# Performance work log

Measured on AMD Instinct MI355X. Metric: run time of the kernel, lower is better.

Reference implementation:

```python
import jax, jax.numpy as jnp
import numpy as np

B, S, D = 2, 2048, 1024
H, HD = 16, 64          # n_heads, head_dim (H*HD == D)
E, K, F = 8, 2, 1024    # n_experts, top_k, expert hidden size
EPS = 1e-6


def setup_inputs() -> dict:
    key = jax.random.key(0)
    ks = jax.random.split(key, 10)
    g = lambda k, shape, sc: jax.random.normal(k, shape, jnp.float32) * sc
    return {
        "x": g(ks[0], (B, S, D), 1.0),
        "attn_norm_w": jnp.ones((D,), jnp.float32),
        "wq": g(ks[1], (D, D), 0.02),
        "wk": g(ks[2], (D, D), 0.02),
        "wv": g(ks[3], (D, D), 0.02),
        "wo": g(ks[4], (D, D), 0.02),
        "ffn_norm_w": jnp.ones((D,), jnp.float32),
        "router_w": g(ks[5], (D, E), 0.02),
        "w1": g(ks[6], (E, D, F), 0.02),  # gate proj per expert
        "w3": g(ks[7], (E, D, F), 0.02),  # up proj per expert
        "w2": g(ks[8], (E, F, D), 0.02),  # down proj per expert
    }


def rmsnorm(x, w):
    return x * jax.lax.rsqrt(jnp.mean(x * x, axis=-1, keepdims=True) + EPS) * w


def attention(x, wq, wk, wv, wo):
    b, s, d = x.shape
    q = (x @ wq).reshape(b, s, H, HD)
    k = (x @ wk).reshape(b, s, H, HD)
    v = (x @ wv).reshape(b, s, H, HD)
    scores = jnp.einsum("bqhd,bkhd->bhqk", q, k) / jnp.sqrt(jnp.float32(HD))
    causal = jnp.tril(jnp.ones((s, s), bool))
    scores = jnp.where(causal, scores, jnp.finfo(scores.dtype).min)
    p = jax.nn.softmax(scores, axis=-1)
    o = jnp.einsum("bhqk,bkhd->bqhd", p, v).reshape(b, s, d)
    return o @ wo


def moe_ffn(x, router_w, w1, w2, w3):
    b, s, d = x.shape
    xt = x.reshape(-1, d)                       # [T, D]
    probs = jax.nn.softmax(xt @ router_w, axis=-1)  # [T, E]
    gate, idx = jax.lax.top_k(probs, K)         # [T, K]
    gate = gate / jnp.sum(gate, axis=-1, keepdims=True)  # renormalize top-k
    T = xt.shape[0]
    combine = jnp.zeros((T, E), xt.dtype).at[jnp.arange(T)[:, None], idx].set(gate)
    out = jnp.zeros_like(xt)
    for e in range(E):  # fixed small loop over experts (dense-equivalent dispatch)
        h = jax.nn.silu(xt @ w1[e]) * (xt @ w3[e])
        out = out + combine[:, e:e + 1] * (h @ w2[e])
    return out.reshape(b, s, d)


def reference(x, attn_norm_w, wq, wk, wv, wo, ffn_norm_w, router_w, w1, w2, w3):
    # h = x + dropout(attn(norm(x)));  out = h + dropout(moe(norm(h)))  (dropout=0)
    h = x + attention(rmsnorm(x, attn_norm_w), wq, wk, wv, wo)
    return h + moe_ffn(rmsnorm(h, ffn_norm_w), router_w, w1, w2, w3)
```

## Files before the change

### kernel.cpp

```cpp
#include <hip/hip_runtime.h>
#include <cstdint>
#include <math.h>

typedef unsigned short u16;
typedef unsigned int u32;
typedef __bf16 bf16x8 __attribute__((ext_vector_type(8)));
typedef float f32x4 __attribute__((ext_vector_type(4)));

#define TBATCH 2
#define TSEQ   2048
#define TDIM   1024
#define THEADS 16
#define THDIM  64
#define TEXP   8
#define TFF    1024
#define TTOK   (TBATCH*TSEQ)
#define TPAIRS (TTOK*2)

__device__ __forceinline__ u16 f2bf(float f) {
  u32 u = __float_as_uint(f);
  u += 0x7FFFu + ((u >> 16) & 1u);
  return (u16)(u >> 16);
}
__device__ __forceinline__ float bf2f(u16 h) { return __uint_as_float(((u32)h) << 16); }

__device__ __forceinline__ void gll16(const void* g, void* l) {
  __builtin_amdgcn_global_load_lds((const __attribute__((address_space(1))) void*)g,
                                   (__attribute__((address_space(3))) void*)l, 16, 0, 0);
}
__device__ __forceinline__ bf16x8 ldsread(const void* p) { return *(const bf16x8*)p; }
__device__ __forceinline__ f32x4 mm16(bf16x8 a, bf16x8 b, f32x4 c) {
  return __builtin_amdgcn_mfma_f32_16x16x32_bf16(a, b, c, 0, 0, 0);
}
__device__ __forceinline__ f32x4 fzero() { f32x4 z = {0.f, 0.f, 0.f, 0.f}; return z; }

__global__ void split_transpose_k(const float* __restrict__ in, u16* __restrict__ outh,
                                  u16* __restrict__ outl, int R, int C) {
  __shared__ float t[32][33];
  const size_t bo = (size_t)blockIdx.z * R * C;
  const int c0 = blockIdx.x * 32, r0 = blockIdx.y * 32;
  const int tx = threadIdx.x, ty = threadIdx.y;
#pragma unroll
  for (int j = 0; j < 32; j += 8)
    t[ty + j][tx] = in[bo + (size_t)(r0 + ty + j) * C + (c0 + tx)];
  __syncthreads();
#pragma unroll
  for (int j = 0; j < 32; j += 8) {
    float v = t[tx][ty + j];
    u16 hv = f2bf(v);
    size_t o = bo + (size_t)(c0 + ty + j) * R + (r0 + tx);
    outh[o] = hv;
    if (outl != nullptr) outl[o] = f2bf(v - bf2f(hv));
  }
}

template<bool SPLIT>
__launch_bounds__(256)
__global__ void rmsnorm_k(const float* __restrict__ x, const float* __restrict__ w,
                          u16* __restrict__ oh, u16* __restrict__ ol) {
  const int t = blockIdx.x, tid = threadIdx.x;
  const float4 xv = ((const float4*)(x + (size_t)t * TDIM))[tid];
  float ss = xv.x*xv.x + xv.y*xv.y + xv.z*xv.z + xv.w*xv.w;
#pragma unroll
  for (int d = 1; d < 64; d <<= 1) ss += __shfl_xor(ss, d, 64);
  __shared__ float sp[4];
  if ((tid & 63) == 0) sp[tid >> 6] = ss;
  __syncthreads();
  const float rsc = rsqrtf((sp[0] + sp[1] + sp[2] + sp[3]) * (1.0f / TDIM) + 1e-6f);
  const float4 wv = ((const float4*)w)[tid];
  float v0 = xv.x*rsc*wv.x, v1 = xv.y*rsc*wv.y, v2 = xv.z*rsc*wv.z, v3 = xv.w*rsc*wv.w;
  u16 h0 = f2bf(v0), h1 = f2bf(v1), h2 = f2bf(v2), h3 = f2bf(v3);
  uint2 ph; ph.x = (u32)h0 | ((u32)h1 << 16); ph.y = (u32)h2 | ((u32)h3 << 16);
  *(uint2*)(oh + (size_t)t * TDIM + tid * 4) = ph;
  if (SPLIT) {
    u16 l0 = f2bf(v0 - bf2f(h0)), l1 = f2bf(v1 - bf2f(h1));
    u16 l2 = f2bf(v2 - bf2f(h2)), l3 = f2bf(v3 - bf2f(h3));
    uint2 pl; pl.x = (u32)l0 | ((u32)l1 << 16); pl.y = (u32)l2 | ((u32)l3 << 16);
    *(uint2*)(ol + (size_t)t * TDIM + tid * 4) = pl;
  }
}

template<int EPI>
__launch_bounds__(256)
__global__ void gemm_x3_k(const u16* __restrict__ Ah, const u16* __restrict__ Al,
                          const u16* __restrict__ Bth, const u16* __restrict__ Btl,
                          u16* __restrict__ outh, u16* __restrict__ outl,
                          float* __restrict__ outf, const float* __restrict__ resid,
                          int M, int N, int K) {
  __shared__ u16 sAh[128 * 32], sAl[128 * 32], sBh[64 * 32], sBl[64 * 32];
  const int tid = threadIdx.x, wid = tid >> 6, lane = tid & 63;
  const int m0 = blockIdx.x * 128, n0 = blockIdx.y * 64;
  const int wr = wid >> 1, wc = wid & 1;

  f32x4 acc[4][2];
#pragma unroll
  for (int i = 0; i < 4; i++)
#pragma unroll
    for (int j = 0; j < 2; j++) acc[i][j] = fzero();

  const int srow = tid >> 2;
  const int scol = (tid & 3) * 8;
  const size_t a0 = (size_t)(m0 + srow) * K + scol;
  const size_t a1 = (size_t)(m0 + srow + 64) * K + scol;
  const size_t b0 = (size_t)(n0 + srow) * K + scol;
  const int ldsw = wid * 1024;

  int aoffs[4], boffs[2];
#pragma unroll
  for (int mf = 0; mf < 4; mf++) aoffs[mf] = (wr*64 + mf*16 + (lane & 15)) * 64 + ((lane >> 4) * 16);
#pragma unroll
  for (int nf = 0; nf < 2; nf++) boffs[nf] = (wc*32 + nf*16 + (lane & 15)) * 64 + ((lane >> 4) * 16);

  const int nk = K >> 5;
  for (int kk = 0; kk < nk; ++kk) {
    const int ke = kk * 32;
    gll16(Ah + a0 + ke, (char*)sAh + ldsw);
    gll16(Ah + a1 + ke, (char*)sAh + 4096 + ldsw);
    gll16(Al + a0 + ke, (char*)sAl + ldsw);
    gll16(Al + a1 + ke, (char*)sAl + 4096 + ldsw);
    gll16(Bth + b0 + ke, (char*)sBh + ldsw);
    gll16(Btl + b0 + ke, (char*)sBl + ldsw);
    __syncthreads();
    bf16x8 fah[4], fal[4], fbh[2], fbl[2];
#pragma unroll
    for (int mf = 0; mf < 4; mf++) { fah[mf] = ldsread((char*)sAh + aoffs[mf]); fal[mf] = ldsread((char*)sAl + aoffs[mf]); }
#pragma unroll
    for (int nf = 0; nf < 2; nf++) { fbh[nf] = ldsread((char*)sBh + boffs[nf]); fbl[nf] = ldsread((char*)sBl + boffs[nf]); }
#pragma unroll
    for (int mf = 0; mf < 4; mf++)
#pragma unroll
      for (int nf = 0; nf < 2; nf++) {
        acc[mf][nf] = mm16(fah[mf], fbh[nf], acc[mf][nf]);
        acc[mf][nf] = mm16(fah[mf], fbl[nf], acc[mf][nf]);
        acc[mf][nf] = mm16(fal[mf], fbh[nf], acc[mf][nf]);
      }
    __syncthreads();
  }

#pragma unroll
  for (int mf = 0; mf < 4; mf++)
#pragma unroll
    for (int nf = 0; nf < 2; nf++)
#pragma unroll
      for (int r = 0; r < 4; r++) {
        const int grow = m0 + wr*64 + mf*16 + ((lane >> 4) * 4) + r;
        const int gcol = n0 + wc*32 + nf*16 + (lane & 15);
        const float v = acc[mf][nf][r];
        if (EPI == 0) {
          const size_t o = (size_t)grow * N + gcol;
          u16 hv = f2bf(v);
          outh[o] = hv; outl[o] = f2bf(v - bf2f(hv));
        } else if (EPI == 1) {
          const int b = grow >> 11, s = grow & (TSEQ - 1);
          const int hh = gcol >> 6, hd = gcol & 63;
          const size_t o = ((size_t)((b * THEADS + hh) * THDIM + hd)) * TSEQ + s;
          u16 hv = f2bf(v);
          outh[o] = hv; outl[o] = f2bf(v - bf2f(hv));
        } else {
          const size_t o = (size_t)grow * N + gcol;
          outf[o] = v + resid[o];
        }
      }
}

__launch_bounds__(256)
__global__ void flash_k(const u16* __restrict__ Qh, const u16* __restrict__ Ql,
                        const u16* __restrict__ Kh, const u16* __restrict__ Kl,
                        const u16* __restrict__ Vth, const u16* __restrict__ Vtl,
                        u16* __restrict__ Oh, u16* __restrict__ Ol) {
  __shared__ u16 sK[2][2][4096];
  __shared__ u16 sV[2][2][4096];
  __shared__ u16 sP[2][4][1024];
  const int tid = threadIdx.x, wid = tid >> 6, lane = tid & 63;
  const int qb = blockIdx.x, bh = blockIdx.y;
  const int b = bh >> 4, h = bh & 15;
  const int srow = tid >> 3;
  const int sxcol = (((lane & 7) ^ ((lane >> 3) & 7)) << 3);
  const int ldsw = wid * 1024;

  bf16x8 fqh[2], fql[2];
  {
    const size_t qbase = ((size_t)(b * TSEQ + qb * 64 + wid * 16 + (lane & 15))) * TDIM + h * 64;
#pragma unroll
    for (int kq = 0; kq < 2; kq++) {
      fqh[kq] = *(const bf16x8*)(Qh + qbase + (kq * 4 + (lane >> 4)) * 8);
      fql[kq] = *(const bf16x8*)(Ql + qbase + (kq * 4 + (lane >> 4)) * 8);
    }
  }

  f32x4 oacc[4];
  float m_run[4], l_run[4];
#pragma unroll
  for (int i = 0; i < 4; i++) { oacc[i] = fzero(); m_run[i] = -INFINITY; l_run[i] = 0.f; }

  const size_t kg0 = ((size_t)(b * TSEQ + srow)) * TDIM + h * 64 + sxcol;
  const size_t kg1 = kg0 + (size_t)32 * TDIM;
  const size_t vg0 = ((size_t)((b * THEADS + h) * THDIM + srow)) * TSEQ + sxcol;
  const size_t vg1 = vg0 + (size_t)32 * TSEQ;

  auto stage = [&](int kb, int bi) {
    const size_t ko = (size_t)kb * 64 * TDIM;
    const size_t vo = (size_t)kb * 64;
    gll16(Kh + kg0 + ko, (char*)sK[bi][0] + ldsw);
    gll16(Kh + kg1 + ko, (char*)sK[bi][0] + 4096 + ldsw);
    gll16(Kl + kg0 + ko, (char*)sK[bi][1] + ldsw);
    gll16(Kl + kg1 + ko, (char*)sK[bi][1] + 4096 + ldsw);
    gll16(Vth + vg0 + vo, (char*)sV[bi][0] + ldsw);
    gll16(Vth + vg1 + vo, (char*)sV[bi][0] + 4096 + ldsw);
    gll16(Vtl + vg0 + vo, (char*)sV[bi][1] + ldsw);
    gll16(Vtl + vg1 + vo, (char*)sV[bi][1] + 4096 + ldsw);
  };

  stage(0, 0);
  asm volatile("s_waitcnt vmcnt(0)" ::: "memory");
  __builtin_amdgcn_s_barrier();

  for (int kb = 0; kb <= qb; ++kb) {
    const int cur = kb & 1;
    if (kb < qb) stage(kb + 1, cur ^ 1);

    f32x4 sc[4];
#pragma unroll
    for (int nf = 0; nf < 4; nf++) {
      f32x4 s = fzero();
      const int krow = nf * 16 + (lane & 15);
#pragma unroll
      for (int kq = 0; kq < 2; kq++) {
        const int off = krow * 128 + (((kq * 4 + (lane >> 4)) ^ (lane & 7)) << 4);
        bf16x8 kfh = ldsread((char*)sK[cur][0] + off);
        bf16x8 kfl = ldsread((char*)sK[cur][1] + off);
        s = mm16(fqh[kq], kfh, s);
        s = mm16(fqh[kq], kfl, s);
        s = mm16(fql[kq], kfh, s);
      }
      sc[nf] = s;
    }

    const int qg = qb * 64 + wid * 16 + ((lane >> 4) * 4);
    float pm[4] = {-INFINITY, -INFINITY, -INFINITY, -INFINITY};
#pragma unroll
    for (int nf = 0; nf < 4; nf++) {
      const int kg = kb * 64 + nf * 16 + (lane & 15);
#pragma unroll
      for (int r = 0; r < 4; r++) {
        float v = sc[nf][r] * 0.125f;
        if (kg > qg + r) v = -INFINITY;
        sc[nf][r] = v;
        pm[r] = fmaxf(pm[r], v);
      }
    }
#pragma unroll
    for (int r = 0; r < 4; r++)
#pragma unroll
      for (int d = 1; d < 16; d <<= 1) pm[r] = fmaxf(pm[r], __shfl_xor(pm[r], d, 64));

    float mn[4], esc[4], rs[4];
#pragma unroll
    for (int r = 0; r < 4; r++) {
      mn[r] = fmaxf(m_run[r], pm[r]);
      esc[r] = __expf(m_run[r] - mn[r]);
      rs[r] = 0.f;
    }
#pragma unroll
    for (int nf = 0; nf < 4; nf++)
#pragma unroll
      for (int r = 0; r < 4; r++) {
        float p = __expf(sc[nf][r] - mn[r]);
        sc[nf][r] = p;
        rs[r] += p;
      }
#pragma unroll
    for (int r = 0; r < 4; r++)
#pragma unroll
      for (int d = 1; d < 16; d <<= 1) rs[r] += __shfl_xor(rs[r], d, 64);
#pragma unroll
    for (int r = 0; r < 4; r++) {
      l_run[r] = l_run[r] * esc[r] + rs[r];
      m_run[r] = mn[r];
    }
#pragma unroll
    for (int nf = 0; nf < 4; nf++)
#pragma unroll
      for (int r = 0; r < 4; r++) oacc[nf][r] *= esc[r];

#pragma unroll
    for (int nf = 0; nf < 4; nf++)
#pragma unroll
      for (int r = 0; r < 4; r++) {
        float p = sc[nf][r];
        u16 ph = f2bf(p);
        const int prow = (lane >> 4) * 4 + r;
        const int pbyte = (prow * 128 + (nf * 16 + (lane & 15)) * 2) ^ ((prow & 7) << 4);
        *(u16*)((char*)sP[0][wid] + pbyte) = ph;
        *(u16*)((char*)sP[1][wid] + pbyte) = f2bf(p - bf2f(ph));
      }

#pragma unroll
    for (int nf = 0; nf < 4; nf++) {
#pragma unroll
      for (int kq = 0; kq < 2; kq++) {
        const int prow = lane & 15;
        const int poff = prow * 128 + (((kq * 4 + (lane >> 4)) ^ (prow & 7)) << 4);
        bf16x8 pah = ldsread((char*)sP[0][wid] + poff);
        bf16x8 pal = ldsread((char*)sP[1][wid] + poff);
        const int vrow = nf * 16 + (lane & 15);
        const int voff = vrow * 128 + (((kq * 4 + (lane >> 4)) ^ (lane & 7)) << 4);
        bf16x8 vfh = ldsread((char*)sV[cur][0] + voff);
        bf16x8 vfl = ldsread((char*)sV[cur][1] + voff);
        oacc[nf] = mm16(pah, vfh, oacc[nf]);
        oacc[nf] = mm16(pah, vfl, oacc[nf]);
        oacc[nf] = mm16(pal, vfh, oacc[nf]);
      }
    }
    asm volatile("s_waitcnt vmcnt(0)" ::: "memory");
    __builtin_amdgcn_s_barrier();
  }

#pragma unroll
  for (int r = 0; r < 4; r++) {
    const float inv = 1.0f / l_run[r];
    const int t = b * TSEQ + qb * 64 + wid * 16 + ((lane >> 4) * 4) + r;
#pragma unroll
    for (int nf = 0; nf < 4; nf++) {
      const float v = oacc[nf][r] * inv;
      const size_t o = (size_t)t * TDIM + h * 64 + nf * 16 + (lane & 15);
      u16 hv = f2bf(v);
      Oh[o] = hv; Ol[o] = f2bf(v - bf2f(hv));
    }
  }
}

__launch_bounds__(256)
__global__ void router_k(const float* __restrict__ hres, const float* __restrict__ wn,
                         const float* __restrict__ rw, int* __restrict__ idx01,
                         float* __restrict__ gate01, int* __restrict__ counts) {
  const int t = blockIdx.x, tid = threadIdx.x;
  const float4 xv = ((const float4*)(hres + (size_t)t * TDIM))[tid];
  float ss = xv.x*xv.x + xv.y*xv.y + xv.z*xv.z + xv.w*xv.w;
#pragma unroll
  for (int d = 1; d < 64; d <<= 1) ss += __shfl_xor(ss, d, 64);
  __shared__ float sp[4];
  __shared__ float sacc[4][8];
  if ((tid & 63) == 0) sp[tid >> 6] = ss;
  __syncthreads();
  const float rsc = rsqrtf((sp[0]+sp[1]+sp[2]+sp[3]) * (1.0f / TDIM) + 1e-6f);
  const float4 wv = ((const float4*)wn)[tid];
  const float x0 = xv.x*rsc*wv.x, x1 = xv.y*rsc*wv.y, x2 = xv.z*rsc*wv.z, x3 = xv.w*rsc*wv.w;
  const float* rp = rw + (size_t)(tid * 4) * TEXP;
  float acc[8];
#pragma unroll
  for (int e = 0; e < 8; e++) acc[e] = x0*rp[e] + x1*rp[8+e] + x2*rp[16+e] + x3*rp[24+e];
#pragma unroll
  for (int e = 0; e < 8; e++)
#pragma unroll
    for (int d = 1; d < 64; d <<= 1) acc[e] += __shfl_xor(acc[e], d, 64);
  if ((tid & 63) == 0)
#pragma unroll
    for (int e = 0; e < 8; e++) sacc[tid >> 6][e] = acc[e];
  __syncthreads();
  if (tid == 0) {
    float lg[8];
#pragma unroll
    for (int e = 0; e < 8; e++) lg[e] = sacc[0][e] + sacc[1][e] + sacc[2][e] + sacc[3][e];
    int i1 = 0;
#pragma unroll
    for (int e = 1; e < 8; e++) if (lg[e] > lg[i1]) i1 = e;
    int i2 = (i1 == 0) ? 1 : 0;
#pragma unroll
    for (int e = 0; e < 8; e++) if (e != i1 && lg[e] > lg[i2]) i2 = e;
    const float g1 = 1.0f / (1.0f + __expf(lg[i2] - lg[i1]));
    idx01[t*2] = i1; idx01[t*2+1] = i2;
    gate01[t*2] = g1; gate01[t*2+1] = 1.0f - g1;
    atomicAdd(&counts[i1], 1);
    atomicAdd(&counts[i2], 1);
  }
}

__global__ void zero8_k(int* counts) { if (threadIdx.x < TEXP) counts[threadIdx.x] = 0; }

__global__ void offsets_k(const int* __restrict__ counts, int* __restrict__ cursor,
                          int* __restrict__ bm_e, int* __restrict__ bm_s0,
                          int* __restrict__ bm_end, int* __restrict__ n_active) {
  if (threadIdx.x != 0 || blockIdx.x != 0) return;
  int off = 0, nb = 0;
  for (int e = 0; e < TEXP; e++) {
    const int c = counts[e];
    cursor[e] = off;
    const int end = off + c;
    for (int mb = 0; mb * 128 < c; mb++) { bm_e[nb] = e; bm_s0[nb] = off + mb * 128; bm_end[nb] = end; nb++; }
    off = end;
  }
  *n_active = nb;
}

__global__ void scatter_k(const int* __restrict__ idx01, int* __restrict__ cursor,
                          int* __restrict__ slot_of, int* __restrict__ perm) {
  const int t = blockIdx.x * 256 + threadIdx.x;
  if (t >= TTOK) return;
#pragma unroll
  for (int k = 0; k < 2; k++) {
    const int e = idx01[t*2+k];
    const int slot = atomicAdd(&cursor[e], 1);
    slot_of[t*2+k] = slot;
    perm[slot] = t;
  }
}

__launch_bounds__(256)
__global__ void moe_gemm1_k(const u16* __restrict__ hn, const u16* __restrict__ w1t,
                            const u16* __restrict__ w3t, const int* __restrict__ perm,
                            const int* __restrict__ bm_e, const int* __restrict__ bm_s0,
                            const int* __restrict__ bm_end, const int* __restrict__ n_active,
                            u16* __restrict__ hbuf) {
  if ((int)blockIdx.x >= *n_active) return;
  __shared__ u16 sA[128 * 32], sB1[64 * 32], sB3[64 * 32];
  const int tid = threadIdx.x, wid = tid >> 6, lane = tid & 63;
  const int e = bm_e[blockIdx.x], slot0 = bm_s0[blockIdx.x], send = bm_end[blockIdx.x];
  const int n0 = blockIdx.y * 64;
  const int wr = wid >> 1, wc = wid & 1;
  const int srow = tid >> 2, scol = (tid & 3) * 8;
  const int sa0 = slot0 + srow, sa1 = slot0 + srow + 64;
  const int ta = (sa0 < send) ? perm[sa0] : 0;
  const int tb2 = (sa1 < send) ? perm[sa1] : 0;
  const size_t a0 = (size_t)ta * TDIM + scol;
  const size_t a1 = (size_t)tb2 * TDIM + scol;
  const size_t bb = (size_t)e * TDIM * TFF + (size_t)(n0 + srow) * TDIM + scol;
  const int ldsw = wid * 1024;
  f32x4 ac1[4][2], ac3[4][2];
#pragma unroll
  for (int i = 0; i < 4; i++)
#pragma unroll
    for (int j = 0; j < 2; j++) { ac1[i][j] = fzero(); ac3[i][j] = fzero(); }
  int aoffs[4], boffs[2];
#pragma unroll
  for (int mf = 0; mf < 4; mf++) aoffs[mf] = (wr*64 + mf*16 + (lane & 15)) * 64 + ((lane >> 4) * 16);
#pragma unroll
  for (int nf = 0; nf < 2; nf++) boffs[nf] = (wc*32 + nf*16 + (lane & 15)) * 64 + ((lane >> 4) * 16);

  for (int kk = 0; kk < 32; ++kk) {
    const int ke = kk * 32;
    gll16(hn + a0 + ke, (char*)sA + ldsw);
    gll16(hn + a1 + ke, (char*)sA + 4096 + ldsw);
    gll16(w1t + bb + ke, (char*)sB1 + ldsw);
    gll16(w3t + bb + ke, (char*)sB3 + ldsw);
    __syncthreads();
    bf16x8 fa[4], f1[2], f3[2];
#pragma unroll
    for (int mf = 0; mf < 4; mf++) fa[mf] = ldsread((char*)sA + aoffs[mf]);
#pragma unroll
    for (int nf = 0; nf < 2; nf++) { f1[nf] = ldsread((char*)sB1 + boffs[nf]); f3[nf] = ldsread((char*)sB3 + boffs[nf]); }
#pragma unroll
    for (int mf = 0; mf < 4; mf++)
#pragma unroll
      for (int nf = 0; nf < 2; nf++) {
        ac1[mf][nf] = mm16(fa[mf], f1[nf], ac1[mf][nf]);
        ac3[mf][nf] = mm16(fa[mf], f3[nf], ac3[mf][nf]);
      }
    __syncthreads();
  }

#pragma unroll
  for (int mf = 0; mf < 4; mf++)
#pragma unroll
    for (int nf = 0; nf < 2; nf++)
#pragma unroll
      for (int r = 0; r < 4; r++) {
        const int slot = slot0 + wr*64 + mf*16 + ((lane >> 4) * 4) + r;
        if (slot < send) {
          const int col = n0 + wc*32 + nf*16 + (lane & 15);
          const float z1 = ac1[mf][nf][r], z3 = ac3[mf][nf][r];
          const float hv = z1 / (1.0f + __expf(-z1)) * z3;
          hbuf[(size_t)slot * TFF + col] = f2bf(hv);
        }
      }
}

__launch_bounds__(256)
__global__ void moe_gemm2_k(const u16* __restrict__ hbuf, const u16* __restrict__ w2t,
                            const int* __restrict__ bm_e, const int* __restrict__ bm_s0,
                            const int* __restrict__ bm_end, const int* __restrict__ n_active,
                            u16* __restrict__ pout) {
  if ((int)blockIdx.x >= *n_active) return;
  __shared__ u16 sA[128 * 32], sB[64 * 32];
  const int tid = threadIdx.x, wid = tid >> 6, lane = tid & 63;
  const int e = bm_e[blockIdx.x], slot0 = bm_s0[blockIdx.x], send = bm_end[blockIdx.x];
  const int n0 = blockIdx.y * 64;
  const int wr = wid >> 1, wc = wid & 1;
  const int srow = tid >> 2, scol = (tid & 3) * 8;
  int sa0 = slot0 + srow; if (sa0 > TPAIRS - 1) sa0 = TPAIRS - 1;
  int sa1 = slot0 + srow + 64; if (sa1 > TPAIRS - 1) sa1 = TPAIRS - 1;
  const size_t a0 = (size_t)sa0 * TFF + scol;
  const size_t a1 = (size_t)sa1 * TFF + scol;
  const size_t bb = (size_t)e * TDIM * TFF + (size_t)(n0 + srow) * TFF + scol;
  const int ldsw = wid * 1024;
  f32x4 acc[4][2];
#pragma unroll
  for (int i = 0; i < 4; i++)
#pragma unroll
    for (int j = 0; j < 2; j++) acc[i][j] = fzero();
  int aoffs[4], boffs[2];
#pragma unroll
  for (int mf = 0; mf < 4; mf++) aoffs[mf] = (wr*64 + mf*16 + (lane & 15)) * 64 + ((lane >> 4) * 16);
#pragma unroll
  for (int nf = 0; nf < 2; nf++) boffs[nf] = (wc*32 + nf*16 + (lane & 15)) * 64 + ((lane >> 4) * 16);

  for (int kk = 0; kk < 32; ++kk) {
    const int ke = kk * 32;
    gll16(hbuf + a0 + ke, (char*)sA + ldsw);
    gll16(hbuf + a1 + ke, (char*)sA + 4096 + ldsw);
    gll16(w2t + bb + ke, (char*)sB + ldsw);
    __syncthreads();
    bf16x8 fa[4], fb[2];
#pragma unroll
    for (int mf = 0; mf < 4; mf++) fa[mf] = ldsread((char*)sA + aoffs[mf]);
#pragma unroll
    for (int nf = 0; nf < 2; nf++) fb[nf] = ldsread((char*)sB + boffs[nf]);
#pragma unroll
    for (int mf = 0; mf < 4; mf++)
#pragma unroll
      for (int nf = 0; nf < 2; nf++)
        acc[mf][nf] = mm16(fa[mf], fb[nf], acc[mf][nf]);
    __syncthreads();
  }

#pragma unroll
  for (int mf = 0; mf < 4; mf++)
#pragma unroll
    for (int nf = 0; nf < 2; nf++)
#pragma unroll
      for (int r = 0; r < 4; r++) {
        const int slot = slot0 + wr*64 + mf*16 + ((lane >> 4) * 4) + r;
        if (slot < send) {
          const int col = n0 + wc*32 + nf*16 + (lane & 15);
          pout[(size_t)slot * TDIM + col] = f2bf(acc[mf][nf][r]);
        }
      }
}

__launch_bounds__(256)
__global__ void combine_k(const float* __restrict__ hres, const u16* __restrict__ pout,
                          const int* __restrict__ slot_of, const float* __restrict__ gate01,
                          float* __restrict__ out) {
  const int t = blockIdx.x, tid = threadIdx.x;
  const int s0 = slot_of[t*2], s1 = slot_of[t*2+1];
  const float g0 = gate01[t*2], g1 = gate01[t*2+1];
  const float4 hv = ((const float4*)(hres + (size_t)t * TDIM))[tid];
  const uint2 u0 = *(const uint2*)(pout + (size_t)s0 * TDIM + tid * 4);
  const uint2 u1 = *(const uint2*)(pout + (size_t)s1 * TDIM + tid * 4);
  float4 o;
  o.x = hv.x + g0 * bf2f((u16)(u0.x & 0xffff)) + g1 * bf2f((u16)(u1.x & 0xffff));
  o.y = hv.y + g0 * bf2f((u16)(u0.x >> 16))    + g1 * bf2f((u16)(u1.x >> 16));
  o.z = hv.z + g0 * bf2f((u16)(u0.y & 0xffff)) + g1 * bf2f((u16)(u1.y & 0xffff));
  o.w = hv.w + g0 * bf2f((u16)(u0.y >> 16))    + g1 * bf2f((u16)(u1.y >> 16));
  ((float4*)(out + (size_t)t * TDIM))[tid] = o;
}

extern "C" void kernel_launch(void* const* d_in, const int* in_sizes, int n_in,
                              void* d_out, int out_size, void* d_ws, size_t ws_size,
                              hipStream_t stream) {
  (void)in_sizes; (void)n_in; (void)out_size; (void)ws_size;
  const float* x   = (const float*)d_in[0];
  const float* anw = (const float*)d_in[1];
  const float* wq  = (const float*)d_in[2];
  const float* wk  = (const float*)d_in[3];
  const float* wv  = (const float*)d_in[4];
  const float* wo  = (const float*)d_in[5];
  const float* fnw = (const float*)d_in[6];
  const float* rw  = (const float*)d_in[7];
  const float* w1  = (const float*)d_in[8];
  const float* w3  = (const float*)d_in[9];
  const float* w2  = (const float*)d_in[10];
  float* out = (float*)d_out;

  char* ws = (char*)d_ws;
  size_t off = 0;
  auto take = [&](size_t bytes) -> char* {
    char* p = ws + off;
    off += (bytes + 255) & ~(size_t)255;
    return p;
  };
  const size_t SZ_W = (size_t)TDIM * TDIM * sizeof(u16);
  const size_t SZ_T = (size_t)TTOK * TDIM * sizeof(u16);
  u16* wqt_h = (u16*)take(SZ_W); u16* wqt_l = (u16*)take(SZ_W);
  u16* wkt_h = (u16*)take(SZ_W); u16* wkt_l = (u16*)take(SZ_W);
  u16* wvt_h = (u16*)take(SZ_W); u16* wvt_l = (u16*)take(SZ_W);
  u16* wot_h = (u16*)take(SZ_W); u16* wot_l = (u16*)take(SZ_W);
  u16* w1t = (u16*)take((size_t)TEXP * TDIM * TFF * sizeof(u16));
  u16* w3t = (u16*)take((size_t)TEXP * TDIM * TFF * sizeof(u16));
  u16* w2t = (u16*)take((size_t)TEXP * TDIM * TFF * sizeof(u16));
  u16* xnh = (u16*)take(SZ_T); u16* xnl = (u16*)take(SZ_T);
  u16* qh  = (u16*)take(SZ_T); u16* ql  = (u16*)take(SZ_T);
  u16* kh  = (u16*)take(SZ_T); u16* kl  = (u16*)take(SZ_T);
  u16* vth = (u16*)take(SZ_T); u16* vtl = (u16*)take(SZ_T);
  float* hres = (float*)take((size_t)TTOK * TDIM * sizeof(float));
  int*   idx01  = (int*)take(TTOK * 2 * 4);
  float* gate01 = (float*)take(TTOK * 2 * 4);
  int*   slot_of = (int*)take(TTOK * 2 * 4);
  int*   perm    = (int*)take(TPAIRS * 4);
  int*   counts  = (int*)take(256);
  int*   cursor  = (int*)take(256);
  int*   bm_e    = (int*)take(96 * 4);
  int*   bm_s0   = (int*)take(96 * 4);
  int*   bm_end  = (int*)take(96 * 4);
  int*   n_act   = (int*)take(256);
  u16* oh = xnh; u16* ol = xnl;
  u16* hn = qh;
  u16* hbuf = kh;
  u16* pout = vth;

  dim3 tb32(32, 8);
  split_transpose_k<<<dim3(32, 32, 1), tb32, 0, stream>>>(wq, wqt_h, wqt_l, TDIM, TDIM);
  split_transpose_k<<<dim3(32, 32, 1), tb32, 0, stream>>>(wk, wkt_h, wkt_l, TDIM, TDIM);
  split_transpose_k<<<dim3(32, 32, 1), tb32, 0, stream>>>(wv, wvt_h, wvt_l, TDIM, TDIM);
  split_transpose_k<<<dim3(32, 32, 1), tb32, 0, stream>>>(wo, wot_h, wot_l, TDIM, TDIM);
  split_transpose_k<<<dim3(32, 32, 8), tb32, 0, stream>>>(w1, w1t, nullptr, TDIM, TFF);
  split_transpose_k<<<dim3(32, 32, 8), tb32, 0, stream>>>(w3, w3t, nullptr, TDIM, TFF);
  split_transpose_k<<<dim3(32, 32, 8), tb32, 0, stream>>>(w2, w2t, nullptr, TFF, TDIM);
  zero8_k<<<1, 64, 0, stream>>>(counts);
  rmsnorm_k<true><<<TTOK, 256, 0, stream>>>(x, anw, xnh, xnl);
  gemm_x3_k<0><<<dim3(TTOK/128, TDIM/64), 256, 0, stream>>>(xnh, xnl, wqt_h, wqt_l, qh, ql, nullptr, nullptr, TTOK, TDIM, TDIM);
  gemm_x3_k<0><<<dim3(TTOK/128, TDIM/64), 256, 0, stream>>>(xnh, xnl, wkt_h, wkt_l, kh, kl, nullptr, nullptr, TTOK, TDIM, TDIM);
  gemm_x3_k<1><<<dim3(TTOK/128, TDIM/64), 256, 0, stream>>>(xnh, xnl, wvt_h, wvt_l, vth, vtl, nullptr, nullptr, TTOK, TDIM, TDIM);
  flash_k<<<dim3(TSEQ/64, TBATCH*THEADS), 256, 0, stream>>>(qh, ql, kh, kl, vth, vtl, oh, ol);
  gemm_x3_k<2><<<dim3(TTOK/128, TDIM/64), 256, 0, stream>>>(oh, ol, wot_h, wot_l, nullptr, nullptr, hres, x, TTOK, TDIM, TDIM);
  rmsnorm_k<false><<<TTOK, 256, 0, stream>>>(hres, fnw, hn, nullptr);
  router_k<<<TTOK, 256, 0, stream>>>(hres, fnw, rw, idx01, gate01, counts);
  offsets_k<<<1, 1, 0, stream>>>(counts, cursor, bm_e, bm_s0, bm_end, n_act);
  scatter_k<<<TTOK/256, 256, 0, stream>>>(idx01, cursor, slot_of, perm);
  moe_gemm1_k<<<dim3(72, TFF/64), 256, 0, stream>>>(hn, w1t, w3t, perm, bm_e, bm_s0, bm_end, n_act, hbuf);
  moe_gemm2_k<<<dim3(72, TDIM/64), 256, 0, stream>>>(hbuf, w2t, bm_e, bm_s0, bm_end, n_act, pout);
  combine_k<<<TTOK, 256, 0, stream>>>(hres, pout, slot_of, gate01, out);
}
```

Baseline: 645.1 us.

## Process two query tiles per flash block, reverse block order, defer row-sum reduction

Each flash-attention block now handles 128 query rows as two 64-row halves that share every staged K/V tile, halving global K/V traffic per query. Blocks are launched in reverse query order so the longest causal rows start first, which should improve tail balance. The per-iteration cross-lane row-sum shuffle is replaced by per-lane partial sums reduced once at the end. The cost is half as many blocks (512), more registers for the doubled accumulators, and one fully masked half on the last K tile.

```diff
diff --git a/kernel.cpp b/kernel.cpp
--- a/kernel.cpp
+++ b/kernel.cpp
@@ -172,26 +172,30 @@
   __shared__ u16 sV[2][2][4096];
   __shared__ u16 sP[2][4][1024];
   const int tid = threadIdx.x, wid = tid >> 6, lane = tid & 63;
-  const int qb = blockIdx.x, bh = blockIdx.y;
+  const int qb = (int)(gridDim.x - 1 - blockIdx.x);
+  const int bh = blockIdx.y;
   const int b = bh >> 4, h = bh & 15;
   const int srow = tid >> 3;
   const int sxcol = (((lane & 7) ^ ((lane >> 3) & 7)) << 3);
   const int ldsw = wid * 1024;
 
-  bf16x8 fqh[2], fql[2];
-  {
-    const size_t qbase = ((size_t)(b * TSEQ + qb * 64 + wid * 16 + (lane & 15))) * TDIM + h * 64;
+  bf16x8 fqh[2][2], fql[2][2];
+#pragma unroll
+  for (int hh = 0; hh < 2; hh++) {
+    const size_t qbase = ((size_t)(b * TSEQ + qb * 128 + hh * 64 + wid * 16 + (lane & 15))) * TDIM + h * 64;
 #pragma unroll
     for (int kq = 0; kq < 2; kq++) {
-      fqh[kq] = *(const bf16x8*)(Qh + qbase + (kq * 4 + (lane >> 4)) * 8);
-      fql[kq] = *(const bf16x8*)(Ql + qbase + (kq * 4 + (lane >> 4)) * 8);
+      fqh[hh][kq] = *(const bf16x8*)(Qh + qbase + (kq * 4 + (lane >> 4)) * 8);
+      fql[hh][kq] = *(const bf16x8*)(Ql + qbase + (kq * 4 + (lane >> 4)) * 8);
     }
   }
 
-  f32x4 oacc[4];
-  float m_run[4], l_run[4];
-#pragma unroll
-  for (int i = 0; i < 4; i++) { oacc[i] = fzero(); m_run[i] = -INFINITY; l_run[i] = 0.f; }
+  f32x4 oacc[2][4];
+  float m_run[2][4], l_lane[2][4];
+#pragma unroll
+  for (int hh = 0; hh < 2; hh++)
+#pragma unroll
+    for (int i = 0; i < 4; i++) { oacc[hh][i] = fzero(); m_run[hh][i] = -INFINITY; l_lane[hh][i] = 0.f; }
 
   const size_t kg0 = ((size_t)(b * TSEQ + srow)) * TDIM + h * 64 + sxcol;
   const size_t kg1 = kg0 + (size_t)32 * TDIM;
@@ -211,105 +215,105 @@
     gll16(Vtl + vg1 + vo, (char*)sV[bi][1] + 4096 + ldsw);
   };
 
+  const int nkb = 2 * qb + 2;
   stage(0, 0);
   asm volatile("s_waitcnt vmcnt(0)" ::: "memory");
   __builtin_amdgcn_s_barrier();
 
-  for (int kb = 0; kb <= qb; ++kb) {
+  for (int kb = 0; kb < nkb; ++kb) {
     const int cur = kb & 1;
-    if (kb < qb) stage(kb + 1, cur ^ 1);
-
-    f32x4 sc[4];
-#pragma unroll
-    for (int nf = 0; nf < 4; nf++) {
-      f32x4 s = fzero();
-      const int krow = nf * 16 + (lane & 15);
-#pragma unroll
-      for (int kq = 0; kq < 2; kq++) {
-        const int off = krow * 128 + (((kq * 4 + (lane >> 4)) ^ (lane & 7)) << 4);
-        bf16x8 kfh = ldsread((char*)sK[cur][0] + off);
-        bf16x8 kfl = ldsread((char*)sK[cur][1] + off);
-        s = mm16(fqh[kq], kfh, s);
-        s = mm16(fqh[kq], kfl, s);
-        s = mm16(fql[kq], kfh, s);
-      }
-      sc[nf] = s;
-    }
-
-    const int qg = qb * 64 + wid * 16 + ((lane >> 4) * 4);
-    float pm[4] = {-INFINITY, -INFINITY, -INFINITY, -INFINITY};
-#pragma unroll
-    for (int nf = 0; nf < 4; nf++) {
-      const int kg = kb * 64 + nf * 16 + (lane & 15);
+    if (kb + 1 < nkb) stage(kb + 1, cur ^ 1);
+
+#pragma unroll
+    for (int hh = 0; hh < 2; hh++) {
+      if (kb * 64 > qb * 128 + hh * 64 + 63) continue;
+
+      f32x4 sc[4];
+#pragma unroll
+      for (int nf = 0; nf < 4; nf++) {
+        f32x4 s = fzero();
+        const int krow = nf * 16 + (lane & 15);
+#pragma unroll
+        for (int kq = 0; kq < 2; kq++) {
+          const int off = krow * 128 + (((kq * 4 + (lane >> 4)) ^ (lane & 7)) << 4);
+          bf16x8 kfh = ldsread((char*)sK[cur][0] + off);
+          bf16x8 kfl = ldsread((char*)sK[cur][1] + off);
+          s = mm16(fqh[hh][kq], kfh, s);
+          s = mm16(fqh[hh][kq], kfl, s);
+          s = mm16(fql[hh][kq], kfh, s);
+        }
+        sc[nf] = s;
+      }
+
+      const int qg = qb * 128 + hh * 64 + wid * 16 + ((lane >> 4) * 4);
+      float pm[4] = {-INFINITY, -INFINITY, -INFINITY, -INFINITY};
+#pragma unroll
+      for (int nf = 0; nf < 4; nf++) {
+        const int kg = kb * 64 + nf * 16 + (lane & 15);
+#pragma unroll
+        for (int r = 0; r < 4; r++) {
+          float v = sc[nf][r] * 0.125f;
+          if (kg > qg + r) v = -INFINITY;
+          sc[nf][r] = v;
+          pm[r] = fmaxf(pm[r], v);
+        }
+      }
+#pragma unroll
+      for (int r = 0; r < 4; r++)
+#pragma unroll
+        for (int d = 1; d < 16; d <<= 1) pm[r] = fmaxf(pm[r], __shfl_xor(pm[r], d, 64));
+
+      float mn[4], esc[4];
 #pragma unroll
       for (int r = 0; r < 4; r++) {
-        float v = sc[nf][r] * 0.125f;
-        if (kg > qg + r) v = -INFINITY;
-        sc[nf][r] = v;
-        pm[r] = fmaxf(pm[r], v);
-      }
-    }
-#pragma unroll
-    for (int r = 0; r < 4; r++)
-#pragma unroll
-      for (int d = 1; d < 16; d <<= 1) pm[r] = fmaxf(pm[r], __shfl_xor(pm[r], d, 64));
-
-    float mn[4], esc[4], rs[4];
-#pragma unroll
-    for (int r = 0; r < 4; r++) {
-      mn[r] = fmaxf(m_run[r], pm[r]);
-      esc[r] = __expf(m_run[r] - mn[r]);
-      rs[r] = 0.f;
-    }
-#pragma unroll
-    for (int nf = 0; nf < 4; nf++)
-#pragma unroll
-      for (int r = 0; r < 4; r++) {
-        float p = __expf(sc[nf][r] - mn[r]);
-        sc[nf][r] = p;
-        rs[r] += p;
-      }
-#pragma unroll
-    for (int r = 0; r < 4; r++)
-#pragma unroll
-      for (int d = 1; d < 16; d <<= 1) rs[r] += __shfl_xor(rs[r], d, 64);
-#pragma unroll
-    for (int r = 0; r < 4; r++) {
-      l_run[r] = l_run[r] * esc[r] + rs[r];
-      m_run[r] = mn[r];
-    }
-#pragma unroll
-    for (int nf = 0; nf < 4; nf++)
-#pragma unroll
-      for (int r = 0; r < 4; r++) oacc[nf][r] *= esc[r];
-
-#pragma unroll
-    for (int nf = 0; nf < 4; nf++)
-#pragma unroll
-      for (int r = 0; r < 4; r++) {
-        float p = sc[nf][r];
-        u16 ph = f2bf(p);
-        const int prow = (lane >> 4) * 4 + r;
-        const int pbyte = (prow * 128 + (nf * 16 + (lane & 15)) * 2) ^ ((prow & 7) << 4);
-        *(u16*)((char*)sP[0][wid] + pbyte) = ph;
-        *(u16*)((char*)sP[1][wid] + pbyte) = f2bf(p - bf2f(ph));
-      }
-
-#pragma unroll
-    for (int nf = 0; nf < 4; nf++) {
-#pragma unroll
-      for (int kq = 0; kq < 2; kq++) {
-        const int prow = lane & 15;
-        const int poff = prow * 128 + (((kq * 4 + (lane >> 4)) ^ (prow & 7)) << 4);
-        bf16x8 pah = ldsread((char*)sP[0][wid] + poff);
-        bf16x8 pal = ldsread((char*)sP[1][wid] + poff);
-        const int vrow = nf * 16 + (lane & 15);
-        const int voff = vrow * 128 + (((kq * 4 + (lane >> 4)) ^ (lane & 7)) << 4);
-        bf16x8 vfh = ldsread((char*)sV[cur][0] + voff);
-        bf16x8 vfl = ldsread((char*)sV[cur][1] + voff);
-        oacc[nf] = mm16(pah, vfh, oacc[nf]);
-        oacc[nf] = mm16(pah, vfl, oacc[nf]);
-        oacc[nf] = mm16(pal, vfh, oacc[nf]);
+        mn[r] = fmaxf(m_run[hh][r], pm[r]);
+        esc[r] = __expf(m_run[hh][r] - mn[r]);
+        m_run[hh][r] = mn[r];
+      }
+      float ls[4] = {0.f, 0.f, 0.f, 0.f};
+#pragma unroll
+      for (int nf = 0; nf < 4; nf++)
+#pragma unroll
+        for (int r = 0; r < 4; r++) {
+          float p = __expf(sc[nf][r] - mn[r]);
+          sc[nf][r] = p;
+          ls[r] += p;
+        }
+#pragma unroll
+      for (int r = 0; r < 4; r++) l_lane[hh][r] = l_lane[hh][r] * esc[r] + ls[r];
+#pragma unroll
+      for (int nf = 0; nf < 4; nf++)
+#pragma unroll
+        for (int r = 0; r < 4; r++) oacc[hh][nf][r] *= esc[r];
+
+#pragma unroll
+      for (int nf = 0; nf < 4; nf++)
+#pragma unroll
+        for (int r = 0; r < 4; r++) {
+          float p = sc[nf][r];
+          u16 ph = f2bf(p);
+          const int prow = (lane >> 4) * 4 + r;
+          const int pbyte = (prow * 128 + (nf * 16 + (lane & 15)) * 2) ^ ((prow & 7) << 4);
+          *(u16*)((char*)sP[0][wid] + pbyte) = ph;
+          *(u16*)((char*)sP[1][wid] + pbyte) = f2bf(p - bf2f(ph));
+        }
+
+#pragma unroll
+      for (int nf = 0; nf < 4; nf++) {
+#pragma unroll
+        for (int kq = 0; kq < 2; kq++) {
+          const int prow = lane & 15;
+          const int poff = prow * 128 + (((kq * 4 + (lane >> 4)) ^ (prow & 7)) << 4);
+          bf16x8 pah = ldsread((char*)sP[0][wid] + poff);
+          bf16x8 pal = ldsread((char*)sP[1][wid] + poff);
+          const int vrow = nf * 16 + (lane & 15);
+          const int voff = vrow * 128 + (((kq * 4 + (lane >> 4)) ^ (lane & 7)) << 4);
+          bf16x8 vfh = ldsread((char*)sV[cur][0] + voff);
+          bf16x8 vfl = ldsread((char*)sV[cur][1] + voff);
+          oacc[hh][nf] = mm16(pah, vfh, oacc[hh][nf]);
+          oacc[hh][nf] = mm16(pah, vfl, oacc[hh][nf]);
+          oacc[hh][nf] = mm16(pal, vfh, oacc[hh][nf]);
+        }
       }
     }
     asm volatile("s_waitcnt vmcnt(0)" ::: "memory");
@@ -317,17 +321,22 @@
   }
 
 #pragma unroll
-  for (int r = 0; r < 4; r++) {
-    const float inv = 1.0f / l_run[r];
-    const int t = b * TSEQ + qb * 64 + wid * 16 + ((lane >> 4) * 4) + r;
-#pragma unroll
-    for (int nf = 0; nf < 4; nf++) {
-      const float v = oacc[nf][r] * inv;
-      const size_t o = (size_t)t * TDIM + h * 64 + nf * 16 + (lane & 15);
-      u16 hv = f2bf(v);
-      Oh[o] = hv; Ol[o] = f2bf(v - bf2f(hv));
+  for (int hh = 0; hh < 2; hh++)
+#pragma unroll
+    for (int r = 0; r < 4; r++) {
+      float lt = l_lane[hh][r];
+#pragma unroll
+      for (int d = 1; d < 16; d <<= 1) lt += __shfl_xor(lt, d, 64);
+      const float inv = 1.0f / lt;
+      const int t = b * TSEQ + qb * 128 + hh * 64 + wid * 16 + ((lane >> 4) * 4) + r;
+#pragma unroll
+      for (int nf = 0; nf < 4; nf++) {
+        const float v = oacc[hh][nf][r] * inv;
+        const size_t o = (size_t)t * TDIM + h * 64 + nf * 16 + (lane & 15);
+        u16 hv = f2bf(v);
+        Oh[o] = hv; Ol[o] = f2bf(v - bf2f(hv));
+      }
     }
-  }
 }
 
 __launch_bounds__(256)
@@ -621,7 +630,7 @@
   gemm_x3_k<0><<<dim3(TTOK/128, TDIM/64), 256, 0, stream>>>(xnh, xnl, wqt_h, wqt_l, qh, ql, nullptr, nullptr, TTOK, TDIM, TDIM);
   gemm_x3_k<0><<<dim3(TTOK/128, TDIM/64), 256, 0, stream>>>(xnh, xnl, wkt_h, wkt_l, kh, kl, nullptr, nullptr, TTOK, TDIM, TDIM);
   gemm_x3_k<1><<<dim3(TTOK/128, TDIM/64), 256, 0, stream>>>(xnh, xnl, wvt_h, wvt_l, vth, vtl, nullptr, nullptr, TTOK, TDIM, TDIM);
-  flash_k<<<dim3(TSEQ/64, TBATCH*THEADS), 256, 0, stream>>>(qh, ql, kh, kl, vth, vtl, oh, ol);
+  flash_k<<<dim3(TSEQ/128, TBATCH*THEADS), 256, 0, stream>>>(qh, ql, kh, kl, vth, vtl, oh, ol);
   gemm_x3_k<2><<<dim3(TTOK/128, TDIM/64), 256, 0, stream>>>(oh, ol, wot_h, wot_l, nullptr, nullptr, hres, x, TTOK, TDIM, TDIM);
   rmsnorm_k<false><<<TTOK, 256, 0, stream>>>(hres, fnw, hn, nullptr);
   router_k<<<TTOK, 256, 0, stream>>>(hres, fnw, rw, idx01, gate01, counts);
```

Result: faster. 621.0 us (-3.7%).

## Load flash K/V fragments directly from global, reverse block order, defer row-sum reduction

Applied to the files above, without the earlier changes.

The flash attention kernel stops staging K and V tiles through double-buffered shared memory with barriers. Each wave now reads its MFMA fragments straight from global memory and relies on the cache for reuse across the four waves. Query blocks are also launched in reverse order so the longest causal blocks start first, and the softmax row-sum cross-lane reduction moves out of the loop to a single final reduction. This removes LDS traffic and per-iteration barriers, but it costs more global/L2 loads per wave with no explicit prefetch, so load latency may be exposed.

```diff
diff --git a/kernel.cpp b/kernel.cpp
--- a/kernel.cpp
+++ b/kernel.cpp
@@ -168,15 +168,11 @@
                         const u16* __restrict__ Kh, const u16* __restrict__ Kl,
                         const u16* __restrict__ Vth, const u16* __restrict__ Vtl,
                         u16* __restrict__ Oh, u16* __restrict__ Ol) {
-  __shared__ u16 sK[2][2][4096];
-  __shared__ u16 sV[2][2][4096];
   __shared__ u16 sP[2][4][1024];
   const int tid = threadIdx.x, wid = tid >> 6, lane = tid & 63;
-  const int qb = blockIdx.x, bh = blockIdx.y;
+  const int qb = (int)(gridDim.x - 1 - blockIdx.x);
+  const int bh = blockIdx.y;
   const int b = bh >> 4, h = bh & 15;
-  const int srow = tid >> 3;
-  const int sxcol = (((lane & 7) ^ ((lane >> 3) & 7)) << 3);
-  const int ldsw = wid * 1024;
 
   bf16x8 fqh[2], fql[2];
   {
@@ -189,46 +185,34 @@
   }
 
   f32x4 oacc[4];
-  float m_run[4], l_run[4];
-#pragma unroll
-  for (int i = 0; i < 4; i++) { oacc[i] = fzero(); m_run[i] = -INFINITY; l_run[i] = 0.f; }
-
-  const size_t kg0 = ((size_t)(b * TSEQ + srow)) * TDIM + h * 64 + sxcol;
-  const size_t kg1 = kg0 + (size_t)32 * TDIM;
-  const size_t vg0 = ((size_t)((b * THEADS + h) * THDIM + srow)) * TSEQ + sxcol;
-  const size_t vg1 = vg0 + (size_t)32 * TSEQ;
-
-  auto stage = [&](int kb, int bi) {
-    const size_t ko = (size_t)kb * 64 * TDIM;
-    const size_t vo = (size_t)kb * 64;
-    gll16(Kh + kg0 + ko, (char*)sK[bi][0] + ldsw);
-    gll16(Kh + kg1 + ko, (char*)sK[bi][0] + 4096 + ldsw);
-    gll16(Kl + kg0 + ko, (char*)sK[bi][1] + ldsw);
-    gll16(Kl + kg1 + ko, (char*)sK[bi][1] + 4096 + ldsw);
-    gll16(Vth + vg0 + vo, (char*)sV[bi][0] + ldsw);
-    gll16(Vth + vg1 + vo, (char*)sV[bi][0] + 4096 + ldsw);
-    gll16(Vtl + vg0 + vo, (char*)sV[bi][1] + ldsw);
-    gll16(Vtl + vg1 + vo, (char*)sV[bi][1] + 4096 + ldsw);
-  };
-
-  stage(0, 0);
-  asm volatile("s_waitcnt vmcnt(0)" ::: "memory");
-  __builtin_amdgcn_s_barrier();
+  float m_run[4], l_lane[4];
+#pragma unroll
+  for (int i = 0; i < 4; i++) { oacc[i] = fzero(); m_run[i] = -INFINITY; l_lane[i] = 0.f; }
+
+  size_t koff[2], voff[2];
+#pragma unroll
+  for (int kq = 0; kq < 2; kq++) {
+    koff[kq] = (size_t)(lane & 15) * TDIM + (kq * 4 + (lane >> 4)) * 8;
+    voff[kq] = (size_t)(lane & 15) * TSEQ + (kq * 4 + (lane >> 4)) * 8;
+  }
+  const u16* kbh = Kh + ((size_t)(b * TSEQ)) * TDIM + h * 64;
+  const u16* kbl = Kl + ((size_t)(b * TSEQ)) * TDIM + h * 64;
+  const u16* vbh = Vth + ((size_t)((b * THEADS + h) * THDIM)) * TSEQ;
+  const u16* vbl = Vtl + ((size_t)((b * THEADS + h) * THDIM)) * TSEQ;
 
   for (int kb = 0; kb <= qb; ++kb) {
-    const int cur = kb & 1;
-    if (kb < qb) stage(kb + 1, cur ^ 1);
+    const size_t kt = (size_t)kb * 64 * TDIM;
+    const size_t vt = (size_t)kb * 64;
 
     f32x4 sc[4];
 #pragma unroll
     for (int nf = 0; nf < 4; nf++) {
       f32x4 s = fzero();
-      const int krow = nf * 16 + (lane & 15);
+      const size_t krow = kt + (size_t)(nf * 16) * TDIM;
 #pragma unroll
       for (int kq = 0; kq < 2; kq++) {
-        const int off = krow * 128 + (((kq * 4 + (lane >> 4)) ^ (lane & 7)) << 4);
-        bf16x8 kfh = ldsread((char*)sK[cur][0] + off);
-        bf16x8 kfl = ldsread((char*)sK[cur][1] + off);
+        bf16x8 kfh = *(const bf16x8*)(kbh + krow + koff[kq]);
+        bf16x8 kfl = *(const bf16x8*)(kbl + krow + koff[kq]);
         s = mm16(fqh[kq], kfh, s);
         s = mm16(fqh[kq], kfl, s);
         s = mm16(fql[kq], kfh, s);
@@ -254,30 +238,24 @@
 #pragma unroll
       for (int d = 1; d < 16; d <<= 1) pm[r] = fmaxf(pm[r], __shfl_xor(pm[r], d, 64));
 
-    float mn[4], esc[4], rs[4];
+    float mn[4], esc[4];
 #pragma unroll
     for (int r = 0; r < 4; r++) {
       mn[r] = fmaxf(m_run[r], pm[r]);
       esc[r] = __expf(m_run[r] - mn[r]);
-      rs[r] = 0.f;
+      m_run[r] = mn[r];
     }
+    float ls[4] = {0.f, 0.f, 0.f, 0.f};
 #pragma unroll
     for (int nf = 0; nf < 4; nf++)
 #pragma unroll
       for (int r = 0; r < 4; r++) {
         float p = __expf(sc[nf][r] - mn[r]);
         sc[nf][r] = p;
-        rs[r] += p;
-      }
-#pragma unroll
-    for (int r = 0; r < 4; r++)
-#pragma unroll
-      for (int d = 1; d < 16; d <<= 1) rs[r] += __shfl_xor(rs[r], d, 64);
-#pragma unroll
-    for (int r = 0; r < 4; r++) {
-      l_run[r] = l_run[r] * esc[r] + rs[r];
-      m_run[r] = mn[r];
-    }
+        ls[r] += p;
+      }
+#pragma unroll
+    for (int r = 0; r < 4; r++) l_lane[r] = l_lane[r] * esc[r] + ls[r];
 #pragma unroll
     for (int nf = 0; nf < 4; nf++)
 #pragma unroll
@@ -297,28 +275,28 @@
 
 #pragma unroll
     for (int nf = 0; nf < 4; nf++) {
+      const size_t vrow = vt + (size_t)(nf * 16) * TSEQ;
 #pragma unroll
       for (int kq = 0; kq < 2; kq++) {
         const int prow = lane & 15;
         const int poff = prow * 128 + (((kq * 4 + (lane >> 4)) ^ (prow & 7)) << 4);
         bf16x8 pah = ldsread((char*)sP[0][wid] + poff);
         bf16x8 pal = ldsread((char*)sP[1][wid] + poff);
-        const int vrow = nf * 16 + (lane & 15);
-        const int voff = vrow * 128 + (((kq * 4 + (lane >> 4)) ^ (lane & 7)) << 4);
-        bf16x8 vfh = ldsread((char*)sV[cur][0] + voff);
-        bf16x8 vfl = ldsread((char*)sV[cur][1] + voff);
+        bf16x8 vfh = *(const bf16x8*)(vbh + vrow + voff[kq]);
+        bf16x8 vfl = *(const bf16x8*)(vbl + vrow + voff[kq]);
         oacc[nf] = mm16(pah, vfh, oacc[nf]);
         oacc[nf] = mm16(pah, vfl, oacc[nf]);
         oacc[nf] = mm16(pal, vfh, oacc[nf]);
       }
     }
-    asm volatile("s_waitcnt vmcnt(0)" ::: "memory");
-    __builtin_amdgcn_s_barrier();
   }
 
 #pragma unroll
   for (int r = 0; r < 4; r++) {
-    const float inv = 1.0f / l_run[r];
+    float lt = l_lane[r];
+#pragma unroll
+    for (int d = 1; d < 16; d <<= 1) lt += __shfl_xor(lt, d, 64);
+    const float inv = 1.0f / lt;
     const int t = b * TSEQ + qb * 64 + wid * 16 + ((lane >> 4) * 4) + r;
 #pragma unroll
     for (int nf = 0; nf < 4; nf++) {
```

Result: slower. 975.3 us (+51.2%).
